# Optimization experiments

Hardware: AMD Instinct MI355X
Metric: run time of the kernel (lower is better)

Reference implementation:

```python
import jax, jax.numpy as jnp
import numpy as np

B, SD, AD, M, MAXC = 65536, 32, 1, 32, 2  # batch, state_dim, action_dim, msg_dim, max_children


def _l2norm(x):
    # F.normalize(x, dim=-1) with eps=1e-12
    return x / jnp.maximum(jnp.linalg.norm(x, axis=-1, keepdims=True), 1e-12)


def _mlp(x, w1, b1, w2, b2, w3, b3):
    # MLPBase: Linear->ReLU->Linear->ReLU->Linear (400/300 hidden)
    h = jax.nn.relu(x @ w1 + b1)
    h = jax.nn.relu(h @ w2 + b2)
    return h @ w3 + b3


def setup_inputs() -> dict:
    key = jax.random.key(0)
    ks = iter(jax.random.split(key, 40))

    def p(shape):
        return jax.random.normal(next(ks), shape, jnp.float32) * 0.05

    inp = {
        "state": jax.random.normal(next(ks), (B, SD), jnp.float32),
        "action": jax.random.normal(next(ks), (B, AD), jnp.float32),
        # CriticUp params
        "up_fc1_w": p((SD + AD, 64)), "up_fc1_b": p((64,)),
        "up_fc2_w": p((64 + M, 64)), "up_fc2_b": p((64,)),
        "up_fc3_w": p((64, M)), "up_fc3_b": p((M,)),
        "att_w": p((9 + SD, M)), "att_b": p((M,)),
    }
    q_in = 12 + M + AD + M   # rel_pos(12) + self_input(msg_dim) + action + msg_down
    m_in = 12 + M + M        # rel_pos(12) + self_input + msg_down
    for n, d, out in (("q1", q_in, 1), ("q2", q_in, 1), ("msg", m_in, M * MAXC)):
        inp[n + "_w1"] = p((d, 400)); inp[n + "_b1"] = p((400,))
        inp[n + "_w2"] = p((400, 300)); inp[n + "_b2"] = p((300,))
        inp[n + "_w3"] = p((300, out)); inp[n + "_b3"] = p((out,))
    return inp


def reference(state, action,
              up_fc1_w, up_fc1_b, up_fc2_w, up_fc2_b, up_fc3_w, up_fc3_b,
              att_w, att_b,
              q1_w1, q1_b1, q1_w2, q1_b2, q1_w3, q1_b3,
              q2_w1, q2_b1, q2_w2, q2_b2, q2_w3, q2_b3,
              msg_w1, msg_b1, msg_w2, msg_b2, msg_w3, msg_b3):
    b = state.shape[0]
    # ---- bottom-up (num_limbs=1: root has no children -> zero child states/messages) ----
    xu = _l2norm(jnp.concatenate([state, action], -1) @ up_fc1_w + up_fc1_b)  # [b,64]
    ch_states = jnp.zeros((b, MAXC, 9 + SD), state.dtype)
    att = jax.nn.softmax(ch_states @ att_w + att_b, axis=-2)                  # [b,MAXC,M]
    m_up = (jnp.zeros((b, MAXC, M), state.dtype) * att).sum(-2)              # [b,M] (zeros)
    h = jnp.tanh(jnp.concatenate([xu, m_up], -1))
    h = jnp.tanh(h @ up_fc2_w + up_fc2_b)
    msg_up = _l2norm(h @ up_fc3_w + up_fc3_b)                                 # [b,M]
    # ---- top-down (root's parent index -1 wraps to itself -> zero relative offsets) ----
    pos = state[:, :3]
    rel = jnp.concatenate([jnp.zeros((b, 6), state.dtype), pos, pos], -1)     # [b,12]
    m_td = jnp.zeros((b, M), state.dtype)                                     # sliced from zero parent_msg
    xum = jnp.concatenate([rel, msg_up, action, m_td], -1)
    x1 = _mlp(xum, q1_w1, q1_b1, q1_w2, q1_b2, q1_w3, q1_b3)                  # [b,1]
    x2 = _mlp(xum, q2_w1, q2_b1, q2_w2, q2_b2, q2_w3, q2_b3)                  # [b,1]
    xm = jnp.tanh(jnp.concatenate([rel, msg_up, m_td], -1))
    msg_down = _l2norm(_mlp(xm, msg_w1, msg_b1, msg_w2, msg_b2, msg_w3, msg_b3))
    del msg_down  # computed per torch forward but unused in single-limb output
    # stack over 1 limb then sum over limb dim == identity
    return (x1, x2)
```

## Files before the change

### kernel.cpp

```cpp
#include <hip/hip_runtime.h>
#include <math.h>


#define BTOT   65536
#define XUM_OFF 655360ull

#define PH_THR  512
#define PH_ROWS 128
#define PH_BLK  (BTOT / PH_ROWS)
#define F1W 0
#define F1B 2112
#define F2W 2176
#define F2B 6272
#define F3W 6336
#define F3B 8384
#define W0_FLOATS 8416

#define ML_THR  1024
#define ML_ROWS 128
#define ML_BLK  (BTOT / ML_ROWS)
#define H1S     440

typedef float  f32x4 __attribute__((ext_vector_type(4)));
typedef __bf16 bf16x8 __attribute__((ext_vector_type(8)));
typedef unsigned short u16x8 __attribute__((ext_vector_type(8)));

__device__ __forceinline__ unsigned short f2b(float f) {
  union { float f; unsigned int u; } v; v.f = f;
  return (unsigned short)((v.u + 0x7fffu + ((v.u >> 16) & 1u)) >> 16);
}
__device__ __forceinline__ float b2f(unsigned short u) {
  union { unsigned int u; float f; } v; v.u = ((unsigned int)u) << 16;
  return v.f;
}
__device__ __forceinline__ f32x4 MFMA(bf16x8 a, bf16x8 b, f32x4 c) {
  return __builtin_amdgcn_mfma_f32_16x16x32_bf16(a, b, c, 0, 0, 0);
}
__device__ __forceinline__ bf16x8 ld8(const unsigned short* p) {
  return __builtin_bit_cast(bf16x8, *(const u16x8*)p);
}
__device__ __forceinline__ float ftanh(float x) {
  float e = __builtin_amdgcn_exp2f(x * 2.885390081777927f);
  return (e - 1.0f) * __builtin_amdgcn_rcpf(e + 1.0f);
}

struct PackP { const float* qp[12]; unsigned short* ws; };

__global__ void pack_weights(PackP P) {
  const int gid = blockIdx.x * 512 + threadIdx.x;
  if (gid >= 624 * 64) return;
  const int lane = gid & 63, f = gid >> 6;
  const int q = f / 312, fl = f - q * 312;
  const float* w1 = P.qp[q * 6 + 0];
  const float* b1 = P.qp[q * 6 + 1];
  const float* w2 = P.qp[q * 6 + 2];
  int nt, ks; const bool isw1 = (fl < 52);
  if (isw1) { nt = fl >> 1; ks = fl & 1; }
  else      { int fl2 = fl - 52; nt = fl2 / 13; ks = fl2 - nt * 13; }
  const int col = nt * 16 + (lane & 15);
  const int k0  = ks * 32 + (lane >> 4) * 8;
  unsigned short v[8];
  #pragma unroll
  for (int j = 0; j < 8; ++j) {
    const int k = k0 + j;
    float x = 0.f;
    if (isw1) {
      if (col < 400) {
        if (k < 39) x = w1[(6 + k) * 400 + col];
        else if (k == 39) x = b1[col];
      }
    } else {
      if (k < 400 && col < 300) x = w2[k * 300 + col];
    }
    v[j] = f2b(x);
  }
  *(u16x8*)(P.ws + (size_t)f * 512 + lane * 8) = *(const u16x8*)v;
}

struct P0 {
  const float* state; const float* action;
  const float* f1w; const float* f1b;
  const float* f2w; const float* f2b;
  const float* f3w; const float* f3b;
  unsigned short* xum;
};

__global__ __launch_bounds__(PH_THR, 4) void phase0_kernel(P0 P) {
  __shared__ float w0[W0_FLOATS];
  __shared__ unsigned short hx[PH_ROWS * 68];
  const int tid = threadIdx.x;
  const int row = tid >> 2, sub = tid & 3, j0 = sub * 16;
  const long grow = (long)blockIdx.x * PH_ROWS + row;

  for (int i = tid; i < 528;  i += PH_THR) *(f32x4*)(w0 + F1W + 4*i) = *(const f32x4*)(P.f1w + 4*i);
  for (int i = tid; i < 16;   i += PH_THR) *(f32x4*)(w0 + F1B + 4*i) = *(const f32x4*)(P.f1b + 4*i);
  for (int i = tid; i < 1024; i += PH_THR) *(f32x4*)(w0 + F2W + 4*i) = *(const f32x4*)(P.f2w + 4*i);
  for (int i = tid; i < 16;   i += PH_THR) *(f32x4*)(w0 + F2B + 4*i) = *(const f32x4*)(P.f2b + 4*i);
  for (int i = tid; i < 512;  i += PH_THR) *(f32x4*)(w0 + F3W + 4*i) = *(const f32x4*)(P.f3w + 4*i);
  for (int i = tid; i < 8;    i += PH_THR) *(f32x4*)(w0 + F3B + 4*i) = *(const f32x4*)(P.f3b + 4*i);

  float sa[33];
  {
    const float4* sp = (const float4*)(P.state + grow * 32);
    #pragma unroll
    for (int c = 0; c < 8; ++c) {
      float4 v = sp[c];
      sa[c*4+0] = v.x; sa[c*4+1] = v.y; sa[c*4+2] = v.z; sa[c*4+3] = v.w;
    }
    sa[32] = P.action[grow];
  }
  __syncthreads();

  float acc[16];
  #pragma unroll
  for (int j = 0; j < 16; ++j) acc[j] = w0[F1B + j0 + j];
  #pragma unroll 4
  for (int i = 0; i < 33; ++i) {
    const float s = sa[i];
    const f32x4* wr = (const f32x4*)&w0[F1W + i * 64 + j0];
    #pragma unroll
    for (int c = 0; c < 4; ++c) {
      f32x4 wv = wr[c];
      acc[c*4+0] += s * wv[0]; acc[c*4+1] += s * wv[1];
      acc[c*4+2] += s * wv[2]; acc[c*4+3] += s * wv[3];
    }
  }
  {
    float ss = 0.f;
    #pragma unroll
    for (int j = 0; j < 16; ++j) ss += acc[j] * acc[j];
    ss += __shfl_xor(ss, 1, 64); ss += __shfl_xor(ss, 2, 64);
    const float sc = 1.f / fmaxf(sqrtf(ss), 1e-12f);
    #pragma unroll
    for (int j = 0; j < 16; ++j) hx[row * 68 + j0 + j] = f2b(ftanh(acc[j] * sc));
  }
  __syncthreads();
  #pragma unroll
  for (int j = 0; j < 16; ++j) acc[j] = w0[F2B + j0 + j];
  #pragma unroll 4
  for (int i = 0; i < 64; ++i) {
    const float hv = b2f(hx[row * 68 + i]);
    const f32x4* wr = (const f32x4*)&w0[F2W + i * 64 + j0];
    #pragma unroll
    for (int c = 0; c < 4; ++c) {
      f32x4 wv = wr[c];
      acc[c*4+0] += hv * wv[0]; acc[c*4+1] += hv * wv[1];
      acc[c*4+2] += hv * wv[2]; acc[c*4+3] += hv * wv[3];
    }
  }
  __syncthreads();
  #pragma unroll
  for (int j = 0; j < 16; ++j) hx[row * 68 + j0 + j] = f2b(ftanh(acc[j]));
  __syncthreads();
  const int j0m = sub * 8;
  float am[8];
  #pragma unroll
  for (int j = 0; j < 8; ++j) am[j] = w0[F3B + j0m + j];
  #pragma unroll 4
  for (int i = 0; i < 64; ++i) {
    const float hv = b2f(hx[row * 68 + i]);
    const f32x4* wr = (const f32x4*)&w0[F3W + i * 32 + j0m];
    #pragma unroll
    for (int c = 0; c < 2; ++c) {
      f32x4 wv = wr[c];
      am[c*4+0] += hv * wv[0]; am[c*4+1] += hv * wv[1];
      am[c*4+2] += hv * wv[2]; am[c*4+3] += hv * wv[3];
    }
  }
  float sm = 0.f;
  #pragma unroll
  for (int j = 0; j < 8; ++j) sm += am[j] * am[j];
  sm += __shfl_xor(sm, 1, 64); sm += __shfl_xor(sm, 2, 64);
  const float scm = 1.f / fmaxf(sqrtf(sm), 1e-12f);
  __syncthreads();
  #pragma unroll
  for (int j = 0; j < 8; ++j) hx[row * 68 + j0m + j] = f2b(am[j] * scm);
  __syncthreads();
  {
    u16x8 v0, v1;
    #pragma unroll
    for (int t = 0; t < 16; ++t) {
      const int c = j0 + t;
      unsigned short u;
      if      (c < 3)  u = f2b(sa[c]);
      else if (c < 6)  u = f2b(sa[c - 3]);
      else if (c < 38) u = hx[row * 68 + (c - 6)];
      else if (c == 38) u = f2b(sa[32]);
      else if (c == 39) u = 0x3f80;
      else              u = 0;
      if (t < 8) v0[t] = u; else v1[t - 8] = u;
    }
    unsigned short* dst = P.xum + (size_t)grow * 64 + j0;
    *(u16x8*)dst = v0;
    *(u16x8*)(dst + 8) = v1;
  }
}

struct P1 {
  const unsigned short* img; const unsigned short* xum;
  const float* q1b2; const float* q1w3; const float* q1b3;
  const float* q2b2; const float* q2w3; const float* q2b3;
  float* out;
};

__global__ __launch_bounds__(ML_THR) void mlp_kernel(P1 P) {
  __shared__ __align__(16) unsigned short h1[ML_ROWS * H1S];
  __shared__ float xred[ML_ROWS * 4];

  const int tid  = threadIdx.x;
  const int lane = tid & 63, w = tid >> 6;
  const int rl = lane & 15, g = lane >> 4;

  const int r1 = w & 7, ch = w >> 3;
  const int wm = w >> 2, wn = w & 3;

  const unsigned short* xr = P.xum + ((size_t)blockIdx.x * ML_ROWS + r1 * 16 + rl) * 64;
  const bf16x8 af0 = ld8(xr + g * 8);
  const bf16x8 af1 = ld8(xr + 32 + g * 8);

  for (int q = 0; q < 2; ++q) {
    {
      const unsigned short* w1f = P.img + ((size_t)(q * 312 + ch * 26)) * 512 + lane * 8;
      for (int t = 0; t < 13; ++t) {
        const bf16x8 b0 = ld8(w1f + (size_t)(t * 2) * 512);
        const bf16x8 b1 = ld8(w1f + (size_t)(t * 2 + 1) * 512);
        f32x4 a = (f32x4){0.f, 0.f, 0.f, 0.f};
        a = MFMA(af0, b0, a);
        a = MFMA(af1, b1, a);
        const int nt = ch * 13 + t;
        #pragma unroll
        for (int i = 0; i < 4; ++i)
          h1[(r1 * 16 + g * 4 + i) * H1S + nt * 16 + rl] = f2b(fmaxf(a[i], 0.f));
      }
    }
    __syncthreads();

    f32x4 acc2[2][5];
    #pragma unroll
    for (int mt = 0; mt < 2; ++mt)
      #pragma unroll
      for (int jn = 0; jn < 5; ++jn) acc2[mt][jn] = (f32x4){0.f, 0.f, 0.f, 0.f};
    {
      const unsigned short* w2f = P.img + ((size_t)(q * 312 + 52 + wn * 5 * 13)) * 512 + lane * 8;
      #pragma unroll 2
      for (int ks = 0; ks < 13; ++ks) {
        const bf16x8 a0 = ld8(&h1[(wm * 32 + rl) * H1S + ks * 32 + g * 8]);
        const bf16x8 a1 = ld8(&h1[(wm * 32 + 16 + rl) * H1S + ks * 32 + g * 8]);
        #pragma unroll
        for (int jn = 0; jn < 5; ++jn) {
          const bf16x8 b = ld8(w2f + (size_t)(jn * 13 + ks) * 512);
          acc2[0][jn] = MFMA(a0, b, acc2[0][jn]);
          acc2[1][jn] = MFMA(a1, b, acc2[1][jn]);
        }
      }
    }

    const float* b2p = q ? P.q2b2 : P.q1b2;
    const float* w3  = q ? P.q2w3 : P.q1w3;
    const float* b3  = q ? P.q2b3 : P.q1b3;
    float xp[2][4];
    #pragma unroll
    for (int mt = 0; mt < 2; ++mt)
      #pragma unroll
      for (int i = 0; i < 4; ++i) xp[mt][i] = 0.f;
    #pragma unroll
    for (int jn = 0; jn < 5; ++jn) {
      const int n = wn * 80 + jn * 16 + rl;
      if (n < 300) {
        const float bv = b2p[n], wv = w3[n];
        #pragma unroll
        for (int mt = 0; mt < 2; ++mt)
          #pragma unroll
          for (int i = 0; i < 4; ++i)
            xp[mt][i] += fmaxf(acc2[mt][jn][i] + bv, 0.f) * wv;
      }
    }
    #pragma unroll
    for (int off = 1; off < 16; off <<= 1)
      #pragma unroll
      for (int mt = 0; mt < 2; ++mt)
        #pragma unroll
        for (int i = 0; i < 4; ++i)
          xp[mt][i] += __shfl_xor(xp[mt][i], off, 64);
    if (rl == 0) {
      #pragma unroll
      for (int mt = 0; mt < 2; ++mt)
        #pragma unroll
        for (int i = 0; i < 4; ++i)
          xred[(wm * 32 + mt * 16 + g * 4 + i) * 4 + wn] = xp[mt][i];
    }
    __syncthreads();
    if (tid < ML_ROWS) {
      const float4 xv = *(const float4*)&xred[tid * 4];
      P.out[(size_t)q * BTOT + (size_t)blockIdx.x * ML_ROWS + tid] =
          xv.x + xv.y + xv.z + xv.w + b3[0];
    }
    __syncthreads();
  }
}

extern "C" void kernel_launch(void* const* d_in, const int* in_sizes, int n_in,
                              void* d_out, int out_size, void* d_ws, size_t ws_size,
                              hipStream_t stream) {
  (void)in_sizes; (void)n_in; (void)out_size; (void)ws_size;
  PackP K;
  for (int i = 0; i < 12; ++i) K.qp[i] = (const float*)d_in[10 + i];
  K.ws = (unsigned short*)d_ws;
  pack_weights<<<dim3(78), dim3(512), 0, stream>>>(K);

  P0 A;
  A.state  = (const float*)d_in[0];
  A.action = (const float*)d_in[1];
  A.f1w = (const float*)d_in[2]; A.f1b = (const float*)d_in[3];
  A.f2w = (const float*)d_in[4]; A.f2b = (const float*)d_in[5];
  A.f3w = (const float*)d_in[6]; A.f3b = (const float*)d_in[7];
  A.xum = (unsigned short*)((unsigned char*)d_ws + XUM_OFF);
  phase0_kernel<<<dim3(PH_BLK), dim3(PH_THR), 0, stream>>>(A);

  P1 B;
  B.img  = (const unsigned short*)d_ws;
  B.xum  = (const unsigned short*)((unsigned char*)d_ws + XUM_OFF);
  B.q1b2 = (const float*)d_in[13]; B.q1w3 = (const float*)d_in[14]; B.q1b3 = (const float*)d_in[15];
  B.q2b2 = (const float*)d_in[19]; B.q2w3 = (const float*)d_in[20]; B.q2b3 = (const float*)d_in[21];
  B.out  = (float*)d_out;
  mlp_kernel<<<dim3(ML_BLK), dim3(ML_THR), 0, stream>>>(B);
}
```

Baseline: 113.5 us.

## Fold weight packing into phase0 launch and pack h1 stores as bf16 pairs

Removes the separate pack_weights launch by adding 78 extra blocks to phase0 that do the packing, so one kernel launch and its gap disappear. In the MLP kernel the first-layer MFMA operands are swapped, which transposes the output fragment so each lane holds four consecutive columns. Those are converted with v_cvt_pk_bf16_f32 and written as a single 8-byte store instead of four scalar stores, and the h1 row stride changes to suit the new access pattern. Phase0's small matvecs now read hx four bf16 values at a time. The main risk is LDS bank conflicts from the new stride and the changed store pattern.

```diff
diff --git a/kernel.cpp b/kernel.cpp
--- a/kernel.cpp
+++ b/kernel.cpp
@@ -5,6 +5,7 @@
 #define BTOT   65536
 #define XUM_OFF 655360ull
 
+#define PK_BLK  78
 #define PH_THR  512
 #define PH_ROWS 128
 #define PH_BLK  (BTOT / PH_ROWS)
@@ -19,11 +20,13 @@
 #define ML_THR  1024
 #define ML_ROWS 128
 #define ML_BLK  (BTOT / ML_ROWS)
-#define H1S     440
+#define H1S     424
 
 typedef float  f32x4 __attribute__((ext_vector_type(4)));
 typedef __bf16 bf16x8 __attribute__((ext_vector_type(8)));
 typedef unsigned short u16x8 __attribute__((ext_vector_type(8)));
+typedef unsigned short u16x4 __attribute__((ext_vector_type(4)));
+typedef unsigned int   u32x2 __attribute__((ext_vector_type(2)));
 
 __device__ __forceinline__ unsigned short f2b(float f) {
   union { float f; unsigned int u; } v; v.f = f;
@@ -42,39 +45,6 @@
 __device__ __forceinline__ float ftanh(float x) {
   float e = __builtin_amdgcn_exp2f(x * 2.885390081777927f);
   return (e - 1.0f) * __builtin_amdgcn_rcpf(e + 1.0f);
-}
-
-struct PackP { const float* qp[12]; unsigned short* ws; };
-
-__global__ void pack_weights(PackP P) {
-  const int gid = blockIdx.x * 512 + threadIdx.x;
-  if (gid >= 624 * 64) return;
-  const int lane = gid & 63, f = gid >> 6;
-  const int q = f / 312, fl = f - q * 312;
-  const float* w1 = P.qp[q * 6 + 0];
-  const float* b1 = P.qp[q * 6 + 1];
-  const float* w2 = P.qp[q * 6 + 2];
-  int nt, ks; const bool isw1 = (fl < 52);
-  if (isw1) { nt = fl >> 1; ks = fl & 1; }
-  else      { int fl2 = fl - 52; nt = fl2 / 13; ks = fl2 - nt * 13; }
-  const int col = nt * 16 + (lane & 15);
-  const int k0  = ks * 32 + (lane >> 4) * 8;
-  unsigned short v[8];
-  #pragma unroll
-  for (int j = 0; j < 8; ++j) {
-    const int k = k0 + j;
-    float x = 0.f;
-    if (isw1) {
-      if (col < 400) {
-        if (k < 39) x = w1[(6 + k) * 400 + col];
-        else if (k == 39) x = b1[col];
-      }
-    } else {
-      if (k < 400 && col < 300) x = w2[k * 300 + col];
-    }
-    v[j] = f2b(x);
-  }
-  *(u16x8*)(P.ws + (size_t)f * 512 + lane * 8) = *(const u16x8*)v;
 }
 
 struct P0 {
@@ -82,6 +52,9 @@
   const float* f1w; const float* f1b;
   const float* f2w; const float* f2b;
   const float* f3w; const float* f3b;
+  const float* q1w1; const float* q1b1; const float* q1w2;
+  const float* q2w1; const float* q2b1; const float* q2w2;
+  unsigned short* ws;
   unsigned short* xum;
 };
 
@@ -89,8 +62,40 @@
   __shared__ float w0[W0_FLOATS];
   __shared__ unsigned short hx[PH_ROWS * 68];
   const int tid = threadIdx.x;
+
+  if (blockIdx.x < PK_BLK) {
+    const int gid = blockIdx.x * PH_THR + tid;
+    const int lane = gid & 63, f = gid >> 6;
+    const int q = f / 312, fl = f - q * 312;
+    const float* w1 = q ? P.q2w1 : P.q1w1;
+    const float* b1 = q ? P.q2b1 : P.q1b1;
+    const float* w2 = q ? P.q2w2 : P.q1w2;
+    int nt, ks; const bool isw1 = (fl < 52);
+    if (isw1) { nt = fl >> 1; ks = fl & 1; }
+    else      { int fl2 = fl - 52; nt = fl2 / 13; ks = fl2 - nt * 13; }
+    const int col = nt * 16 + (lane & 15);
+    const int k0  = ks * 32 + (lane >> 4) * 8;
+    unsigned short v[8];
+    #pragma unroll
+    for (int j = 0; j < 8; ++j) {
+      const int k = k0 + j;
+      float x = 0.f;
+      if (isw1) {
+        if (col < 400) {
+          if (k < 39) x = w1[(6 + k) * 400 + col];
+          else if (k == 39) x = b1[col];
+        }
+      } else {
+        if (k < 400 && col < 300) x = w2[k * 300 + col];
+      }
+      v[j] = f2b(x);
+    }
+    *(u16x8*)(P.ws + (size_t)f * 512 + lane * 8) = *(const u16x8*)v;
+    return;
+  }
+
   const int row = tid >> 2, sub = tid & 3, j0 = sub * 16;
-  const long grow = (long)blockIdx.x * PH_ROWS + row;
+  const long grow = (long)(blockIdx.x - PK_BLK) * PH_ROWS + row;
 
   for (int i = tid; i < 528;  i += PH_THR) *(f32x4*)(w0 + F1W + 4*i) = *(const f32x4*)(P.f1w + 4*i);
   for (int i = tid; i < 16;   i += PH_THR) *(f32x4*)(w0 + F1B + 4*i) = *(const f32x4*)(P.f1b + 4*i);
@@ -138,14 +143,18 @@
   #pragma unroll
   for (int j = 0; j < 16; ++j) acc[j] = w0[F2B + j0 + j];
   #pragma unroll 4
-  for (int i = 0; i < 64; ++i) {
-    const float hv = b2f(hx[row * 68 + i]);
-    const f32x4* wr = (const f32x4*)&w0[F2W + i * 64 + j0];
-    #pragma unroll
-    for (int c = 0; c < 4; ++c) {
-      f32x4 wv = wr[c];
-      acc[c*4+0] += hv * wv[0]; acc[c*4+1] += hv * wv[1];
-      acc[c*4+2] += hv * wv[2]; acc[c*4+3] += hv * wv[3];
+  for (int i0 = 0; i0 < 16; ++i0) {
+    const u16x4 hv4 = *(const u16x4*)&hx[row * 68 + i0 * 4];
+    #pragma unroll
+    for (int u = 0; u < 4; ++u) {
+      const float hv = b2f(hv4[u]);
+      const f32x4* wr = (const f32x4*)&w0[F2W + (i0 * 4 + u) * 64 + j0];
+      #pragma unroll
+      for (int c = 0; c < 4; ++c) {
+        f32x4 wv = wr[c];
+        acc[c*4+0] += hv * wv[0]; acc[c*4+1] += hv * wv[1];
+        acc[c*4+2] += hv * wv[2]; acc[c*4+3] += hv * wv[3];
+      }
     }
   }
   __syncthreads();
@@ -157,14 +166,18 @@
   #pragma unroll
   for (int j = 0; j < 8; ++j) am[j] = w0[F3B + j0m + j];
   #pragma unroll 4
-  for (int i = 0; i < 64; ++i) {
-    const float hv = b2f(hx[row * 68 + i]);
-    const f32x4* wr = (const f32x4*)&w0[F3W + i * 32 + j0m];
-    #pragma unroll
-    for (int c = 0; c < 2; ++c) {
-      f32x4 wv = wr[c];
-      am[c*4+0] += hv * wv[0]; am[c*4+1] += hv * wv[1];
-      am[c*4+2] += hv * wv[2]; am[c*4+3] += hv * wv[3];
+  for (int i0 = 0; i0 < 16; ++i0) {
+    const u16x4 hv4 = *(const u16x4*)&hx[row * 68 + i0 * 4];
+    #pragma unroll
+    for (int u = 0; u < 4; ++u) {
+      const float hv = b2f(hv4[u]);
+      const f32x4* wr = (const f32x4*)&w0[F3W + (i0 * 4 + u) * 32 + j0m];
+      #pragma unroll
+      for (int c = 0; c < 2; ++c) {
+        f32x4 wv = wr[c];
+        am[c*4+0] += hv * wv[0]; am[c*4+1] += hv * wv[1];
+        am[c*4+2] += hv * wv[2]; am[c*4+3] += hv * wv[3];
+      }
     }
   }
   float sm = 0.f;
@@ -221,16 +234,21 @@
   for (int q = 0; q < 2; ++q) {
     {
       const unsigned short* w1f = P.img + ((size_t)(q * 312 + ch * 26)) * 512 + lane * 8;
+      unsigned short* h1w = &h1[(size_t)(r1 * 16 + rl) * H1S + ch * 208 + g * 4];
+      #pragma unroll 4
       for (int t = 0; t < 13; ++t) {
         const bf16x8 b0 = ld8(w1f + (size_t)(t * 2) * 512);
         const bf16x8 b1 = ld8(w1f + (size_t)(t * 2 + 1) * 512);
         f32x4 a = (f32x4){0.f, 0.f, 0.f, 0.f};
-        a = MFMA(af0, b0, a);
-        a = MFMA(af1, b1, a);
-        const int nt = ch * 13 + t;
-        #pragma unroll
-        for (int i = 0; i < 4; ++i)
-          h1[(r1 * 16 + g * 4 + i) * H1S + nt * 16 + rl] = f2b(fmaxf(a[i], 0.f));
+        a = MFMA(b0, af0, a);
+        a = MFMA(b1, af1, a);
+        const float c0 = fmaxf(a[0], 0.f), c1 = fmaxf(a[1], 0.f);
+        const float c2 = fmaxf(a[2], 0.f), c3 = fmaxf(a[3], 0.f);
+        unsigned int p01, p23;
+        asm("v_cvt_pk_bf16_f32 %0, %1, %2" : "=v"(p01) : "v"(c0), "v"(c1));
+        asm("v_cvt_pk_bf16_f32 %0, %1, %2" : "=v"(p23) : "v"(c2), "v"(c3));
+        u32x2 pk; pk[0] = p01; pk[1] = p23;
+        *(u32x2*)(h1w + t * 16) = pk;
       }
     }
     __syncthreads();
@@ -241,11 +259,11 @@
       #pragma unroll
       for (int jn = 0; jn < 5; ++jn) acc2[mt][jn] = (f32x4){0.f, 0.f, 0.f, 0.f};
     {
-      const unsigned short* w2f = P.img + ((size_t)(q * 312 + 52 + wn * 5 * 13)) * 512 + lane * 8;
+      const unsigned short* w2f = P.img + ((size_t)(q * 312 + 52 + wn * 65)) * 512 + lane * 8;
       #pragma unroll 2
       for (int ks = 0; ks < 13; ++ks) {
-        const bf16x8 a0 = ld8(&h1[(wm * 32 + rl) * H1S + ks * 32 + g * 8]);
-        const bf16x8 a1 = ld8(&h1[(wm * 32 + 16 + rl) * H1S + ks * 32 + g * 8]);
+        const bf16x8 a0 = ld8(&h1[(size_t)(wm * 32 + rl) * H1S + ks * 32 + g * 8]);
+        const bf16x8 a1 = ld8(&h1[(size_t)(wm * 32 + 16 + rl) * H1S + ks * 32 + g * 8]);
         #pragma unroll
         for (int jn = 0; jn < 5; ++jn) {
           const bf16x8 b = ld8(w2f + (size_t)(jn * 13 + ks) * 512);
@@ -303,19 +321,17 @@
                               void* d_out, int out_size, void* d_ws, size_t ws_size,
                               hipStream_t stream) {
   (void)in_sizes; (void)n_in; (void)out_size; (void)ws_size;
-  PackP K;
-  for (int i = 0; i < 12; ++i) K.qp[i] = (const float*)d_in[10 + i];
-  K.ws = (unsigned short*)d_ws;
-  pack_weights<<<dim3(78), dim3(512), 0, stream>>>(K);
-
   P0 A;
   A.state  = (const float*)d_in[0];
   A.action = (const float*)d_in[1];
   A.f1w = (const float*)d_in[2]; A.f1b = (const float*)d_in[3];
   A.f2w = (const float*)d_in[4]; A.f2b = (const float*)d_in[5];
   A.f3w = (const float*)d_in[6]; A.f3b = (const float*)d_in[7];
+  A.q1w1 = (const float*)d_in[10]; A.q1b1 = (const float*)d_in[11]; A.q1w2 = (const float*)d_in[12];
+  A.q2w1 = (const float*)d_in[16]; A.q2b1 = (const float*)d_in[17]; A.q2w2 = (const float*)d_in[18];
+  A.ws  = (unsigned short*)d_ws;
   A.xum = (unsigned short*)((unsigned char*)d_ws + XUM_OFF);
-  phase0_kernel<<<dim3(PH_BLK), dim3(PH_THR), 0, stream>>>(A);
+  phase0_kernel<<<dim3(PK_BLK + PH_BLK), dim3(PH_THR), 0, stream>>>(A);
 
   P1 B;
   B.img  = (const unsigned short*)d_ws;
```

Measured after the change: 112.2 us. No clear change (-1.1%).
